# Kernel tuning notes

Measured on AMD Instinct MI355X. Metric: run time of the kernel, lower is better.

## Reference

```python
import jax, jax.numpy as jnp
import numpy as np

WIN = 4          # ka_win_num (2x2 grid of windows)
KS = 3           # kernel_size
HEADS = 8
PAD = 1


def setup_inputs() -> dict:
    key = jax.random.key(0)
    ks = jax.random.split(key, 11)
    B, res, C = 8, 256, 64
    c16 = C // 16  # SE bottleneck (dim >= 64 branch)
    inp = {
        "x": jax.random.normal(ks[0], (B, res * res, C), dtype=jnp.float32),
        # per-window grouped-conv weights (the "kernels" fed to attention)
        "conv_w": jax.random.normal(ks[1], (WIN, C, C, KS, KS), dtype=jnp.float32) * 0.05,
        "qkv_w": jax.random.normal(ks[2], (C, 3 * C), dtype=jnp.float32) * 0.05,
        "qkv_b": jax.random.normal(ks[3], (3 * C,), dtype=jnp.float32) * 0.01,
        "proj_w": jax.random.normal(ks[4], (C, C), dtype=jnp.float32) * 0.05,
        "proj_b": jax.random.normal(ks[5], (C,), dtype=jnp.float32) * 0.01,
        # per-window SE params (1x1 convs on pooled (k,k))
        "se_w1": jax.random.normal(ks[6], (WIN, c16, C), dtype=jnp.float32) * 0.1,
        "se_b1": jax.random.normal(ks[7], (WIN, c16), dtype=jnp.float32) * 0.01,
        "se_w2": jax.random.normal(ks[8], (WIN, C, c16), dtype=jnp.float32) * 0.1,
        "se_b2": jax.random.normal(ks[9], (WIN, C), dtype=jnp.float32) * 0.01,
    }
    return inp


def reference(x, conv_w, qkv_w, qkv_b, proj_w, proj_b, se_w1, se_b1, se_w2, se_b2):
    B, L, C = x.shape
    H = int(round(np.sqrt(L)))
    g = int(round(np.sqrt(WIN)))      # windows per side = 2
    ws = H // g                       # window_size
    hd = C // HEADS
    scale = hd ** (-0.5)
    S = WIN * KS * KS                 # attention sequence length

    xw = x.reshape(B, g, ws, g, ws, C).transpose(1, 3, 0, 5, 2, 4)
    xw = xw.reshape(WIN, B, C, ws, ws)

    # ---- gather conv kernels as tokens: weight.view(out,in,k2).permute(0,2,1), concat over windows
    kern_tok = conv_w.reshape(WIN, C, C, KS * KS).transpose(1, 0, 3, 2).reshape(C, S, C)

    # ---- self-attention over kernel tokens (batch = C_out = dim)
    qkv = kern_tok @ qkv_w + qkv_b                                    # (C, S, 3C)
    qkv = qkv.reshape(C, S, 3, HEADS, hd).transpose(2, 0, 3, 1, 4)     # (3, C, H, S, hd)
    q, kk, v = qkv[0] * scale, qkv[1], qkv[2]
    attn = jax.nn.softmax(jnp.einsum('chsd,chtd->chst', q, kk), axis=-1)
    out = jnp.einsum('chst,chtd->chsd', attn, v)                       # (C, H, S, hd)
    out = out.transpose(0, 2, 1, 3).reshape(C, S, C)
    out = out @ proj_w + proj_b

    kern = out.reshape(C, WIN, KS, KS, C).transpose(1, 0, 4, 2, 3)

    # ---- SE over each window's kernel, treating (C_out, C_in, k, k) as (N, Ch, H, W)
    pool = kern.mean(axis=(-2, -1))
    h = jax.nn.relu(jnp.einsum('wnc,wdc->wnd', pool, se_w1) + se_b1[:, None, :])
    s = jax.nn.sigmoid(jnp.einsum('wnd,wcd->wnc', h, se_w2) + se_b2[:, None, :])
    kern = kern * s[..., None, None]

    def conv(xi, wi):
        return jax.lax.conv_general_dilated(xi, wi, (1, 1), [(PAD, PAD), (PAD, PAD)])

    y = jax.vmap(conv)(xw, kern)

    y = y.reshape(g, g, B, C, ws, ws).transpose(2, 0, 4, 1, 5, 3).reshape(B, H * H, C)
    return y
```

## Files before the change

kernel.cpp:

```cpp
#include <hip/hip_runtime.h>
#include <hip/hip_bf16.h>

typedef __bf16 bf16x8 __attribute__((ext_vector_type(8)));
typedef float  f32x4  __attribute__((ext_vector_type(4)));

__global__ __launch_bounds__(192) void qkv_kernel(
    const float* __restrict__ conv_w, const float* __restrict__ qkv_w,
    const float* __restrict__ qkv_b,
    float* __restrict__ qv, float* __restrict__ kvv, float* __restrict__ vv)
{
    __shared__ float tok[64];
    const int bid = blockIdx.x;
    const int co = bid / 36, s = bid - co * 36;
    const int w = s / 9, p = s - w * 9;
    const int t = threadIdx.x;
    if (t < 64) tok[t] = conv_w[(((w * 64 + co) * 64 + t) * 9) + p];
    __syncthreads();
    float acc = qkv_b[t];
#pragma unroll 8
    for (int ci = 0; ci < 64; ++ci) acc += tok[ci] * qkv_w[ci * 192 + t];
    const int trip = t >> 6, rem = t & 63, h = rem >> 3, d = rem & 7;
    if (trip == 0) acc *= 0.35355339059327373f;
    float* dst = (trip == 0) ? qv : ((trip == 1) ? kvv : vv);
    dst[((co * 8 + h) * 36 + s) * 8 + d] = acc;
}

__global__ __launch_bounds__(64) void attn_kernel(
    const float* __restrict__ qv, const float* __restrict__ kvv,
    const float* __restrict__ vv, float* __restrict__ ao)
{
    __shared__ float kl[288], vl[288];
    const int bid = blockIdx.x;
    const int t = threadIdx.x;
    const float* kb = kvv + bid * 288;
    const float* vb = vv + bid * 288;
    for (int i = t; i < 288; i += 64) { kl[i] = kb[i]; vl[i] = vb[i]; }
    __syncthreads();
    if (t < 36) {
        float q[8];
        const float* qb = qv + bid * 288 + t * 8;
#pragma unroll
        for (int d = 0; d < 8; ++d) q[d] = qb[d];
        float sc[36];
        float mx = -1e30f;
#pragma unroll
        for (int u = 0; u < 36; ++u) {
            float a = 0.f;
#pragma unroll
            for (int d = 0; d < 8; ++d) a += q[d] * kl[u * 8 + d];
            sc[u] = a;
            mx = fmaxf(mx, a);
        }
        float sum = 0.f;
        float o[8] = {0.f,0.f,0.f,0.f,0.f,0.f,0.f,0.f};
#pragma unroll
        for (int u = 0; u < 36; ++u) {
            float e = expf(sc[u] - mx);
            sum += e;
#pragma unroll
            for (int d = 0; d < 8; ++d) o[d] += e * vl[u * 8 + d];
        }
        const float inv = 1.0f / sum;
        const int co = bid >> 3, h = bid & 7;
        float* dst = ao + (co * 36 + t) * 64 + h * 8;
#pragma unroll
        for (int d = 0; d < 8; ++d) dst[d] = o[d] * inv;
    }
}

__global__ __launch_bounds__(64) void proj_se_kernel(
    const float* __restrict__ ao, const float* __restrict__ proj_w,
    const float* __restrict__ proj_b,
    const float* __restrict__ se_w1, const float* __restrict__ se_b1,
    const float* __restrict__ se_w2, const float* __restrict__ se_b2,
    ushort* __restrict__ kout)
{
    __shared__ float al[9][64];
    __shared__ float pool[64];
    __shared__ float hb[4];
    const int bid = blockIdx.x;
    const int w = bid >> 6, co = bid & 63;
    const int t = threadIdx.x;
    for (int i = t; i < 576; i += 64) {
        int p = i >> 6, j = i & 63;
        al[p][j] = ao[(co * 36 + w * 9 + p) * 64 + j];
    }
    __syncthreads();
    float kv[9];
#pragma unroll
    for (int p = 0; p < 9; ++p) {
        float a = proj_b[t];
#pragma unroll 8
        for (int j = 0; j < 64; ++j) a += al[p][j] * proj_w[j * 64 + t];
        kv[p] = a;
    }
    float pl = 0.f;
#pragma unroll
    for (int p = 0; p < 9; ++p) pl += kv[p];
    pool[t] = pl * (1.0f / 9.0f);
    __syncthreads();
    if (t < 4) {
        float hh = se_b1[w * 4 + t];
#pragma unroll 8
        for (int c = 0; c < 64; ++c) hh += pool[c] * se_w1[(w * 4 + t) * 64 + c];
        hb[t] = fmaxf(hh, 0.0f);
    }
    __syncthreads();
    float z = se_b2[w * 64 + t];
#pragma unroll
    for (int d = 0; d < 4; ++d) z += hb[d] * se_w2[(w * 64 + t) * 4 + d];
    const float sg = 1.0f / (1.0f + expf(-z));
    const int hhalf = t >> 5, ci32 = t & 31;
#pragma unroll
    for (int p = 0; p < 9; ++p) {
        __hip_bfloat16 hv = __float2bfloat16(kv[p] * sg);
        kout[(((hhalf * 4 + w) * 9) + p) * 2048 + co * 32 + ci32] = *(const ushort*)&hv;
    }
}

__global__ __launch_bounds__(256, 3) void conv_kernel(
    const float* __restrict__ x, const ushort* __restrict__ kern,
    float* __restrict__ out)
{
    __shared__ alignas(16) ushort in_lds[18 * 18 * 64];
    __shared__ alignas(16) ushort kn_lds[3 * 2048];

    const int tid = threadIdx.x;

    const int bid = blockIdx.x;
    const int nb  = ((bid & 7) << 8) + (bid >> 3);
    const int bz  = nb >> 6;
    const int rem = nb & 63;
    const int i0  = (rem >> 3) << 4;
    const int j0  = (rem & 7) << 4;
    const int w = bz >> 3, b = bz & 7;
    const int gi = w >> 1, gj = w & 1;

    const int wv   = tid >> 6;
    const int lane = tid & 63;
    const int l15  = lane & 15;
    const int hi4  = lane >> 4;

    const char* kern_b = (const char*)kern;
    const int ksrc = (lane << 4) ^ (((lane >> 3) & 3) << 4);
    auto stage_kern = [&](int s, int buf) {
        const int p = s >> 1, hh = s & 1;
        const char* gs = kern_b + ((size_t)((((hh * 4 + w) * 9)) + p) << 12);
        __builtin_amdgcn_global_load_lds(
            (const __attribute__((address_space(1))) unsigned int*)(gs + (wv << 10) + ksrc),
            (__attribute__((address_space(3))) unsigned int*)
                ((char*)kn_lds + (buf << 12) + (wv << 10)),
            16, 0, 0);
    };

    stage_kern(0, 0);
    stage_kern(1, 1);

    {
        const int cc = (tid & 15) << 2;
        const int p0 = tid >> 4;
        float4 v[21];
        unsigned okm = 0;
#pragma unroll
        for (int k = 0; k < 21; ++k) {
            const int pp = p0 + (k << 4);
            const int ppc = pp < 323 ? pp : 323;
            const int r = ppc / 18, q = ppc - r * 18;
            const int iy = i0 - 1 + r, jx = j0 - 1 + q;
            const bool ok = (pp < 324) & (iy >= 0) & (iy < 128) & (jx >= 0) & (jx < 128);
            const int iyc = iy < 0 ? 0 : (iy > 127 ? 127 : iy);
            const int jxc = jx < 0 ? 0 : (jx > 127 ? 127 : jx);
            const size_t xi = (((size_t)b << 16) +
                               (size_t)(gi * 128 + iyc) * 256 + (size_t)(gj * 128 + jxc)) * 64 + cc;
            v[k] = *(const float4*)(x + xi);
            okm |= (unsigned)ok << k;
        }
#pragma unroll
        for (int k = 0; k < 21; ++k) {
            const int pp = p0 + (k << 4);
            if (pp < 324) {
                const int r = pp / 18, q = pp - r * 18;
                float4 z = (okm >> k) & 1 ? v[k] : make_float4(0.f, 0.f, 0.f, 0.f);
                union { ushort4 u; ushort h4[4]; } tmp;
                __hip_bfloat16 b0 = __float2bfloat16(z.x); tmp.h4[0] = *(const ushort*)&b0;
                __hip_bfloat16 b1 = __float2bfloat16(z.y); tmp.h4[1] = *(const ushort*)&b1;
                __hip_bfloat16 b2 = __float2bfloat16(z.z); tmp.h4[2] = *(const ushort*)&b2;
                __hip_bfloat16 b3 = __float2bfloat16(z.w); tmp.h4[3] = *(const ushort*)&b3;
                *(ushort4*)((char*)in_lds +
                    ((pp << 7) + ((cc << 1) ^ ((q & 7) << 4)))) = tmp.u;
            }
        }
    }

    f32x4 acc[4][4];
#pragma unroll
    for (int mf = 0; mf < 4; ++mf)
#pragma unroll
        for (int nf = 0; nf < 4; ++nf)
            acc[mf][nf] = (f32x4){0.f, 0.f, 0.f, 0.f};

    __syncthreads();

#pragma unroll
    for (int s = 0; s < 18; ++s) {
        if (s < 17) asm volatile("s_waitcnt vmcnt(1)" ::: "memory");
        else        asm volatile("s_waitcnt vmcnt(0)" ::: "memory");
        __builtin_amdgcn_sched_barrier(0);
        __builtin_amdgcn_s_barrier();
        __builtin_amdgcn_sched_barrier(0);

        if (s < 16) stage_kern(s + 2, (s + 2) % 3);

        const int buf = s % 3;
        const int p = s >> 1, hh = s & 1;
        const int kh = p / 3, kw = p - kh * 3;

        bf16x8 Kf[4];
#pragma unroll
        for (int nf = 0; nf < 4; ++nf) {
            const int co = nf * 16 + l15;
            Kf[nf] = *(const bf16x8*)((const char*)kn_lds +
                      ((buf << 12) + (co << 6) +
                       ((hi4 << 4) ^ (((co >> 1) & 3) << 4))));
        }

        const int q = l15 + kw;
        const int swz = (q & 7) << 4;
        const int c2 = (hh << 6) | (hi4 << 4);
#pragma unroll
        for (int mf = 0; mf < 4; ++mf) {
            const int r = wv * 4 + mf + kh;
            bf16x8 Af = *(const bf16x8*)((const char*)in_lds +
                          (((r * 18 + q) << 7) + (c2 ^ swz)));
#pragma unroll
            for (int nf = 0; nf < 4; ++nf)
                acc[mf][nf] = __builtin_amdgcn_mfma_f32_16x16x32_bf16(
                    Kf[nf], Af, acc[mf][nf], 0, 0, 0);
        }
    }

    asm volatile("s_waitcnt lgkmcnt(0)" ::: "memory");
    __builtin_amdgcn_sched_barrier(0);
    __builtin_amdgcn_s_barrier();
    __builtin_amdgcn_sched_barrier(0);

    char* ep = (char*)in_lds + (wv << 12);
#pragma unroll
    for (int mf = 0; mf < 4; ++mf) {
        const int iloc = wv * 4 + mf;
        const size_t rowoff = ((size_t)b << 16) +
                              (size_t)(gi * 128 + i0 + iloc) * 256 + (size_t)(gj * 128 + j0);
#pragma unroll
        for (int nf = 0; nf < 4; ++nf) {
            const int off = (nf * 64 + hi4 * 16) ^ ((l15 & 7) << 4);
            *(f32x4*)(ep + l15 * 256 + off) = acc[mf][nf];
        }
#pragma unroll
        for (int t = 0; t < 4; ++t) {
            const int px = t * 4 + hi4;
            f32x4 vv4 = *(const f32x4*)(ep + px * 256 + ((l15 << 4) ^ ((px & 7) << 4)));
            *(f32x4*)(out + (rowoff + px) * 64 + l15 * 4) = vv4;
        }
    }
}

extern "C" void kernel_launch(void* const* d_in, const int* in_sizes, int n_in,
                              void* d_out, int out_size, void* d_ws, size_t ws_size,
                              hipStream_t stream)
{
    const float* x      = (const float*)d_in[0];
    const float* conv_w = (const float*)d_in[1];
    const float* qkv_w  = (const float*)d_in[2];
    const float* qkv_b  = (const float*)d_in[3];
    const float* proj_w = (const float*)d_in[4];
    const float* proj_b = (const float*)d_in[5];
    const float* se_w1  = (const float*)d_in[6];
    const float* se_b1  = (const float*)d_in[7];
    const float* se_w2  = (const float*)d_in[8];
    const float* se_b2  = (const float*)d_in[9];
    float* out = (float*)d_out;

    float* qv = (float*)d_ws;
    float* kv = qv + 147456;
    float* vv = kv + 147456;
    float* ao = vv + 147456;
    ushort* kb = (ushort*)(ao + 147456);

    hipLaunchKernelGGL(qkv_kernel, dim3(2304), dim3(192), 0, stream,
                       conv_w, qkv_w, qkv_b, qv, kv, vv);
    hipLaunchKernelGGL(attn_kernel, dim3(512), dim3(64), 0, stream, qv, kv, vv, ao);
    hipLaunchKernelGGL(proj_se_kernel, dim3(256), dim3(64), 0, stream,
                       ao, proj_w, proj_b, se_w1, se_b1, se_w2, se_b2, kb);
    hipLaunchKernelGGL(conv_kernel, dim3(2048), dim3(256), 0, stream, x, kb, out);
}
```

Before: 83.39 us.

## Fuse QKV, attention, projection and SE into one per-channel kernel

Replaces the three small pre-conv kernels (QKV projection, attention, proj+SE) with a single kernel using one 256-thread block per output channel. All intermediates (tokens, QKV, attention output, projected kernels) stay in LDS, with the QKV and proj weights staged there as well. This removes two kernel launches and the global-memory round trips through the workspace. In exchange, the grid shrinks to 64 blocks with a large LDS footprint, so far fewer CUs run the weight-generation stage in parallel.

```diff
diff --git a/kernel.cpp b/kernel.cpp
--- a/kernel.cpp
+++ b/kernel.cpp
@@ -4,117 +4,114 @@
 typedef __bf16 bf16x8 __attribute__((ext_vector_type(8)));
 typedef float  f32x4  __attribute__((ext_vector_type(4)));
 
-__global__ __launch_bounds__(192) void qkv_kernel(
+__global__ __launch_bounds__(256) void fused_small_kernel(
     const float* __restrict__ conv_w, const float* __restrict__ qkv_w,
-    const float* __restrict__ qkv_b,
-    float* __restrict__ qv, float* __restrict__ kvv, float* __restrict__ vv)
-{
-    __shared__ float tok[64];
-    const int bid = blockIdx.x;
-    const int co = bid / 36, s = bid - co * 36;
-    const int w = s / 9, p = s - w * 9;
-    const int t = threadIdx.x;
-    if (t < 64) tok[t] = conv_w[(((w * 64 + co) * 64 + t) * 9) + p];
-    __syncthreads();
-    float acc = qkv_b[t];
-#pragma unroll 8
-    for (int ci = 0; ci < 64; ++ci) acc += tok[ci] * qkv_w[ci * 192 + t];
-    const int trip = t >> 6, rem = t & 63, h = rem >> 3, d = rem & 7;
-    if (trip == 0) acc *= 0.35355339059327373f;
-    float* dst = (trip == 0) ? qv : ((trip == 1) ? kvv : vv);
-    dst[((co * 8 + h) * 36 + s) * 8 + d] = acc;
-}
-
-__global__ __launch_bounds__(64) void attn_kernel(
-    const float* __restrict__ qv, const float* __restrict__ kvv,
-    const float* __restrict__ vv, float* __restrict__ ao)
-{
-    __shared__ float kl[288], vl[288];
-    const int bid = blockIdx.x;
-    const int t = threadIdx.x;
-    const float* kb = kvv + bid * 288;
-    const float* vb = vv + bid * 288;
-    for (int i = t; i < 288; i += 64) { kl[i] = kb[i]; vl[i] = vb[i]; }
-    __syncthreads();
-    if (t < 36) {
-        float q[8];
-        const float* qb = qv + bid * 288 + t * 8;
-#pragma unroll
-        for (int d = 0; d < 8; ++d) q[d] = qb[d];
-        float sc[36];
-        float mx = -1e30f;
-#pragma unroll
-        for (int u = 0; u < 36; ++u) {
-            float a = 0.f;
-#pragma unroll
-            for (int d = 0; d < 8; ++d) a += q[d] * kl[u * 8 + d];
-            sc[u] = a;
-            mx = fmaxf(mx, a);
-        }
-        float sum = 0.f;
-        float o[8] = {0.f,0.f,0.f,0.f,0.f,0.f,0.f,0.f};
-#pragma unroll
-        for (int u = 0; u < 36; ++u) {
-            float e = expf(sc[u] - mx);
-            sum += e;
-#pragma unroll
-            for (int d = 0; d < 8; ++d) o[d] += e * vl[u * 8 + d];
-        }
-        const float inv = 1.0f / sum;
-        const int co = bid >> 3, h = bid & 7;
-        float* dst = ao + (co * 36 + t) * 64 + h * 8;
-#pragma unroll
-        for (int d = 0; d < 8; ++d) dst[d] = o[d] * inv;
-    }
-}
-
-__global__ __launch_bounds__(64) void proj_se_kernel(
-    const float* __restrict__ ao, const float* __restrict__ proj_w,
+    const float* __restrict__ qkv_b,  const float* __restrict__ proj_w,
     const float* __restrict__ proj_b,
     const float* __restrict__ se_w1, const float* __restrict__ se_b1,
     const float* __restrict__ se_w2, const float* __restrict__ se_b2,
     ushort* __restrict__ kout)
 {
-    __shared__ float al[9][64];
-    __shared__ float pool[64];
-    __shared__ float hb[4];
-    const int bid = blockIdx.x;
-    const int w = bid >> 6, co = bid & 63;
-    const int t = threadIdx.x;
-    for (int i = t; i < 576; i += 64) {
-        int p = i >> 6, j = i & 63;
-        al[p][j] = ao[(co * 36 + w * 9 + p) * 64 + j];
-    }
-    __syncthreads();
-    float kv[9];
-#pragma unroll
-    for (int p = 0; p < 9; ++p) {
-        float a = proj_b[t];
+    __shared__ float tok[36][64];
+    __shared__ float qkvw[64 * 192];
+    __shared__ float qkvl[36][192];
+    __shared__ float aol[36][64];
+    __shared__ float pool[4][64];
+    __shared__ float hb[4][4];
+
+    const int co = blockIdx.x;
+    const int t  = threadIdx.x;
+
+    {
+        const int w = t >> 6, ci = t & 63;
+        const float* src = conv_w + (((w * 64 + co) * 64 + ci) * 9);
+#pragma unroll
+        for (int p = 0; p < 9; ++p) tok[w * 9 + p][ci] = src[p];
+    }
+    for (int i = t; i < 12288; i += 256) qkvw[i] = qkv_w[i];
+    __syncthreads();
+
+    for (int idx = t; idx < 6912; idx += 256) {
+        const int s = idx / 192, d = idx - s * 192;
+        float a = qkv_b[d];
 #pragma unroll 8
-        for (int j = 0; j < 64; ++j) a += al[p][j] * proj_w[j * 64 + t];
-        kv[p] = a;
-    }
-    float pl = 0.f;
-#pragma unroll
-    for (int p = 0; p < 9; ++p) pl += kv[p];
-    pool[t] = pl * (1.0f / 9.0f);
-    __syncthreads();
-    if (t < 4) {
-        float hh = se_b1[w * 4 + t];
+        for (int ci = 0; ci < 64; ++ci) a += tok[s][ci] * qkvw[ci * 192 + d];
+        if (d < 64) a *= 0.35355339059327373f;
+        qkvl[s][d] = a;
+    }
+    __syncthreads();
+
+    {
+        const int h = t >> 5, l = t & 31;
+        for (int qi = l; qi < 36; qi += 32) {
+            float q[8];
+#pragma unroll
+            for (int d = 0; d < 8; ++d) q[d] = qkvl[qi][h * 8 + d];
+            float sc[36];
+            float mx = -1e30f;
+#pragma unroll
+            for (int u = 0; u < 36; ++u) {
+                float a = 0.f;
+#pragma unroll
+                for (int d = 0; d < 8; ++d) a += q[d] * qkvl[u][64 + h * 8 + d];
+                sc[u] = a;
+                mx = fmaxf(mx, a);
+            }
+            float sum = 0.f;
+            float o[8] = {0.f,0.f,0.f,0.f,0.f,0.f,0.f,0.f};
+#pragma unroll
+            for (int u = 0; u < 36; ++u) {
+                float e = expf(sc[u] - mx);
+                sum += e;
+#pragma unroll
+                for (int d = 0; d < 8; ++d) o[d] += e * qkvl[u][128 + h * 8 + d];
+            }
+            const float inv = 1.0f / sum;
+#pragma unroll
+            for (int d = 0; d < 8; ++d) aol[qi][h * 8 + d] = o[d] * inv;
+        }
+    }
+    __syncthreads();
+
+    for (int i = t; i < 4096; i += 256) qkvw[i] = proj_w[i];
+    __syncthreads();
+    for (int idx = t; idx < 2304; idx += 256) {
+        const int s = idx >> 6, j = idx & 63;
+        float a = proj_b[j];
 #pragma unroll 8
-        for (int c = 0; c < 64; ++c) hh += pool[c] * se_w1[(w * 4 + t) * 64 + c];
-        hb[t] = fmaxf(hh, 0.0f);
-    }
-    __syncthreads();
-    float z = se_b2[w * 64 + t];
-#pragma unroll
-    for (int d = 0; d < 4; ++d) z += hb[d] * se_w2[(w * 64 + t) * 4 + d];
-    const float sg = 1.0f / (1.0f + expf(-z));
-    const int hhalf = t >> 5, ci32 = t & 31;
-#pragma unroll
-    for (int p = 0; p < 9; ++p) {
-        __hip_bfloat16 hv = __float2bfloat16(kv[p] * sg);
-        kout[(((hhalf * 4 + w) * 9) + p) * 2048 + co * 32 + ci32] = *(const ushort*)&hv;
+        for (int d = 0; d < 64; ++d) a += aol[s][d] * qkvw[d * 64 + j];
+        tok[s][j] = a;
+    }
+    __syncthreads();
+
+    {
+        const int w = t >> 6, ci = t & 63;
+        float pl = 0.f;
+#pragma unroll
+        for (int p = 0; p < 9; ++p) pl += tok[w * 9 + p][ci];
+        pool[w][ci] = pl * (1.0f / 9.0f);
+    }
+    __syncthreads();
+    if (t < 16) {
+        const int w = t >> 2, d = t & 3;
+        float hh = se_b1[w * 4 + d];
+#pragma unroll 8
+        for (int c = 0; c < 64; ++c) hh += pool[w][c] * se_w1[(w * 4 + d) * 64 + c];
+        hb[w][d] = fmaxf(hh, 0.0f);
+    }
+    __syncthreads();
+    {
+        const int w = t >> 6, ci = t & 63;
+        float z = se_b2[w * 64 + ci];
+#pragma unroll
+        for (int d = 0; d < 4; ++d) z += hb[w][d] * se_w2[(w * 64 + ci) * 4 + d];
+        const float sg = 1.0f / (1.0f + expf(-z));
+        const int hh2 = ci >> 5, ci32 = ci & 31;
+#pragma unroll
+        for (int p = 0; p < 9; ++p) {
+            __hip_bfloat16 hv = __float2bfloat16(tok[w * 9 + p][ci] * sg);
+            kout[(((hh2 * 4 + w) * 9) + p) * 2048 + co * 32 + ci32] = *(const ushort*)&hv;
+        }
     }
 }
 
@@ -280,16 +277,10 @@
     const float* se_b2  = (const float*)d_in[9];
     float* out = (float*)d_out;
 
-    float* qv = (float*)d_ws;
-    float* kv = qv + 147456;
-    float* vv = kv + 147456;
-    float* ao = vv + 147456;
-    ushort* kb = (ushort*)(ao + 147456);
-
-    hipLaunchKernelGGL(qkv_kernel, dim3(2304), dim3(192), 0, stream,
-                       conv_w, qkv_w, qkv_b, qv, kv, vv);
-    hipLaunchKernelGGL(attn_kernel, dim3(512), dim3(64), 0, stream, qv, kv, vv, ao);
-    hipLaunchKernelGGL(proj_se_kernel, dim3(256), dim3(64), 0, stream,
-                       ao, proj_w, proj_b, se_w1, se_b1, se_w2, se_b2, kb);
+    ushort* kb = (ushort*)d_ws;
+
+    hipLaunchKernelGGL(fused_small_kernel, dim3(64), dim3(256), 0, stream,
+                       conv_w, qkv_w, qkv_b, proj_w, proj_b,
+                       se_w1, se_b1, se_w2, se_b2, kb);
     hipLaunchKernelGGL(conv_kernel, dim3(2048), dim3(256), 0, stream, x, kb, out);
 }
```

Result: slower. 123.6 us (+48.2%).
